# Kernel optimization log

Measured on AMD Instinct MI355X. Metric: run time of the kernel, lower is better.

Reference implementation:

```python
import jax, jax.numpy as jnp
import numpy as np

N_NODES = 20000
N_EDGES = 320000
N_GRAPHS = 64
F_IN = 128
HID = 128
K = 3
LEAK = 0.01  # nn.LeakyReLU default negative_slope


def _glorot(key, shape):
    fan_in, fan_out = shape[-2], shape[-1]
    s = jnp.sqrt(2.0 / (fan_in + fan_out))
    return jax.random.normal(key, shape, dtype=jnp.float32) * s


def setup_inputs() -> dict:
    key = jax.random.key(0)
    ks = jax.random.split(key, 12)
    x = jax.random.normal(ks[0], (N_NODES, F_IN), dtype=jnp.float32)
    edge_index = jax.random.randint(ks[1], (2, N_EDGES), 0, N_NODES, dtype=jnp.int64)
    batch = jnp.sort(jax.random.randint(ks[2], (N_NODES,), 0, N_GRAPHS, dtype=jnp.int64))
    # K-hop GraphConv weights: (K+1) matrices per layer
    W1 = _glorot(ks[3], (K + 1, F_IN, HID));       b1 = jnp.zeros((HID,), jnp.float32)
    W2 = _glorot(ks[4], (K + 1, HID, 2 * HID));    b2 = jnp.zeros((2 * HID,), jnp.float32)
    W3 = _glorot(ks[5], (K + 1, 2 * HID, 4 * HID)); b3 = jnp.zeros((4 * HID,), jnp.float32)
    # classifier MLP
    Wm1 = _glorot(ks[6], (4 * HID, 1024)); bm1 = jnp.zeros((1024,), jnp.float32)
    Wm2 = _glorot(ks[7], (1024, 512));     bm2 = jnp.zeros((512,), jnp.float32)
    Wm3 = _glorot(ks[8], (512, 4));        bm3 = jnp.zeros((4,), jnp.float32)
    return dict(x=x, edge_index=edge_index, batch=batch,
                W1=W1, b1=b1, W2=W2, b2=b2, W3=W3, b3=b3,
                Wm1=Wm1, bm1=bm1, Wm2=Wm2, bm2=bm2, Wm3=Wm3, bm3=bm3)


def _khop_conv(x, src, dst, W, b):
    # out = sum_{k=0..K} (A^k x) W_k + b, A = scatter-sum of src features onto dst
    h = x
    out = h @ W[0]
    for k in range(1, W.shape[0]):
        h = jax.ops.segment_sum(h[src], dst, num_segments=N_NODES)  # one hop
        out = out + h @ W[k]
    return out + b


def reference(x, edge_index, batch, W1, b1, W2, b2, W3, b3, Wm1, bm1, Wm2, bm2, Wm3, bm3):
    src, dst = edge_index[0], edge_index[1]
    h = _khop_conv(x, src, dst, W1, b1)
    h = jnp.where(h > 0, h, LEAK * h)
    h = _khop_conv(h, src, dst, W2, b2)
    h = jnp.where(h > 0, h, LEAK * h)
    h = _khop_conv(h, src, dst, W3, b3)
    # global max pool per graph -> [N_GRAPHS, 4*HID]
    g = jax.ops.segment_max(h, batch, num_segments=N_GRAPHS)
    # classifier head
    g = jax.nn.relu(g @ Wm1 + bm1)
    g = jax.nn.relu(g @ Wm2 + bm2)
    return g @ Wm3 + bm3
```

## Files before the change

kernel.cpp:

```cpp
#include <hip/hip_runtime.h>
#include <stdint.h>

#define NN 20000
#define NNP 20096
#define NE 320000
#define NG 64

typedef unsigned short u16;
typedef __attribute__((ext_vector_type(8))) short short8;
typedef __attribute__((ext_vector_type(4))) float f32x4;

__device__ __forceinline__ void glds16(const void* g, const void* l) {
    __builtin_amdgcn_global_load_lds((const __attribute__((address_space(1))) void*)g,
                                     (__attribute__((address_space(3))) void*)l, 16, 0, 0);
}

__device__ __forceinline__ u16 f2bf(float f) {
    unsigned u = __float_as_uint(f);
    return (u16)((u + 0x7FFFu + ((u >> 16) & 1u)) >> 16);
}

__global__ void hist_kernel(const int* __restrict__ dst, int* __restrict__ cnt, int E) {
    int i = blockIdx.x * blockDim.x + threadIdx.x;
    if (i < E) atomicAdd(&cnt[dst[i]], 1);
}

__global__ void scan_kernel(const int* __restrict__ cnt, int* __restrict__ rp, int n) {
    __shared__ int part[1024];
    int tid = threadIdx.x;
    const int CH = (n + 1023) / 1024;
    int base = tid * CH;
    int s = 0;
    for (int i = 0; i < CH; i++) { int idx = base + i; if (idx < n) s += cnt[idx]; }
    part[tid] = s;
    __syncthreads();
    for (int off = 1; off < 1024; off <<= 1) {
        int v = (tid >= off) ? part[tid - off] : 0;
        __syncthreads();
        part[tid] += v;
        __syncthreads();
    }
    int run = (tid == 0) ? 0 : part[tid - 1];
    for (int i = 0; i < CH; i++) {
        int idx = base + i;
        if (idx < n) { rp[idx] = run; run += cnt[idx]; }
    }
    if (tid == 1023) rp[n] = part[1023];
}

__global__ void copy_int(const int* __restrict__ a, int* __restrict__ b, int n) {
    int i = blockIdx.x * blockDim.x + threadIdx.x;
    if (i < n) b[i] = a[i];
}

__global__ void scatter_kernel(const int* __restrict__ src, const int* __restrict__ dstv,
                               int* __restrict__ ofs, int* __restrict__ col, int E) {
    int i = blockIdx.x * blockDim.x + threadIdx.x;
    if (i < E) {
        int p = atomicAdd(&ofs[dstv[i]], 1);
        col[p] = src[i];
    }
}

__global__ void conv_x(const float* __restrict__ x, u16* __restrict__ S1) {
    int i = blockIdx.x * blockDim.x + threadIdx.x;
    if (i >= NN * 128 / 8) return;
    int row = i >> 4, c = (i & 15) * 8;
    const float* p = x + (size_t)row * 128 + c;
    uint4 r;
    unsigned* pr = (unsigned*)&r;
#pragma unroll
    for (int j = 0; j < 4; j++)
        pr[j] = (unsigned)f2bf(p[2 * j]) | ((unsigned)f2bf(p[2 * j + 1]) << 16);
    *(uint4*)(S1 + (size_t)row * 512 + c) = r;
}

__global__ void convT(const float* __restrict__ W, u16* __restrict__ WT, int K, int M) {
    __shared__ float tile[32][33];
    int m0 = blockIdx.x * 32, k0 = blockIdx.y * 32;
    int tx = threadIdx.x & 31, ty = threadIdx.x >> 5;
#pragma unroll
    for (int i = 0; i < 32; i += 8)
        tile[ty + i][tx] = W[(size_t)(k0 + ty + i) * M + m0 + tx];
    __syncthreads();
#pragma unroll
    for (int i = 0; i < 32; i += 8)
        WT[(size_t)(m0 + ty + i) * K + k0 + tx] = f2bf(tile[tx][ty + i]);
}

__global__ void g2bf(const unsigned* __restrict__ genc, u16* __restrict__ gb) {
    int i = blockIdx.x * blockDim.x + threadIdx.x;
    if (i >= NG * 512) return;
    unsigned u = genc[i];
    u = (u & 0x80000000u) ? (u ^ 0x80000000u) : ~u;
    gb[i] = f2bf(__uint_as_float(u));
}

__global__ __launch_bounds__(256) void prop_win(
    const int* __restrict__ rp, const int* __restrict__ col,
    u16* __restrict__ S, int stride, int in_off, int out_off) {
    int win = blockIdx.x;
    int node = blockIdx.y * 64 + (threadIdx.x >> 2);
    int c = (threadIdx.x & 3) * 8;
    if (node >= NN) return;
    int s0 = rp[node], s1 = rp[node + 1];
    const u16* base = S + in_off + win * 32 + c;
    float acc[8] = {};
    auto accum = [&](uint4 v) {
        const unsigned* pv = (const unsigned*)&v;
#pragma unroll
        for (int j = 0; j < 4; j++) {
            acc[2 * j]     += __uint_as_float(pv[j] << 16);
            acc[2 * j + 1] += __uint_as_float(pv[j] & 0xFFFF0000u);
        }
    };
    int e = s0;
    for (; e + 4 <= s1; e += 4) {
        int i0 = col[e], i1 = col[e + 1], i2 = col[e + 2], i3 = col[e + 3];
        uint4 v0 = *(const uint4*)(base + (size_t)i0 * stride);
        uint4 v1 = *(const uint4*)(base + (size_t)i1 * stride);
        uint4 v2 = *(const uint4*)(base + (size_t)i2 * stride);
        uint4 v3 = *(const uint4*)(base + (size_t)i3 * stride);
        accum(v0); accum(v1); accum(v2); accum(v3);
    }
    for (; e < s1; e++)
        accum(*(const uint4*)(base + (size_t)col[e] * stride));
    uint4 r;
    unsigned* pr = (unsigned*)&r;
#pragma unroll
    for (int j = 0; j < 4; j++)
        pr[j] = (unsigned)f2bf(acc[2 * j]) | ((unsigned)f2bf(acc[2 * j + 1]) << 16);
    *(uint4*)(S + (size_t)node * stride + out_off + win * 32 + c) = r;
}

template <int TM, int EPI, int ACT>
__global__ __launch_bounds__(256) void gemm_bf16(
    const u16* __restrict__ A, int lda, const u16* __restrict__ BT,
    int Kp, int M, const float* __restrict__ bias,
    u16* __restrict__ outB, int ldo,
    unsigned* __restrict__ genc, const int* __restrict__ batch) {
    __shared__ u16 Al[TM * 32];
    __shared__ u16 Bl[128 * 32];
    __shared__ unsigned gbuf[EPI == 1 ? 256 : 4];
    constexpr int MR = TM / 32;
    int col0 = blockIdx.x * 128, row0 = blockIdx.y * TM;
    int t = threadIdx.x;
    int w = t >> 6, ln = t & 63;
    int wm = (w >> 1) * (TM / 2), wn = (w & 1) * 64;
    int srowB = w * 32 + (ln >> 2);
    int srowA = (TM == 128) ? srowB : (w * 16 + (ln >> 2));
    int skc = (ln & 3) * 8;
    f32x4 acc[MR][4] = {};

    if (EPI == 1) gbuf[t] = 0;

    for (int k0 = 0; k0 < Kp; k0 += 32) {
        if (TM == 128) {
            glds16(A + (size_t)(row0 + srowA) * lda + k0 + skc,      &Al[w * 1024]);
            glds16(A + (size_t)(row0 + srowA + 16) * lda + k0 + skc, &Al[w * 1024 + 512]);
        } else {
            glds16(A + (size_t)(row0 + srowA) * lda + k0 + skc,      &Al[w * 512]);
        }
        glds16(BT + (size_t)(col0 + srowB) * Kp + k0 + skc,          &Bl[w * 1024]);
        glds16(BT + (size_t)(col0 + srowB + 16) * Kp + k0 + skc,     &Bl[w * 1024 + 512]);
        __syncthreads();
        short8 af[MR], bf[4];
#pragma unroll
        for (int m = 0; m < MR; m++)
            af[m] = *(const short8*)&Al[(wm + m * 16 + (ln & 15)) * 32 + (ln >> 4) * 8];
#pragma unroll
        for (int n = 0; n < 4; n++)
            bf[n] = *(const short8*)&Bl[(wn + n * 16 + (ln & 15)) * 32 + (ln >> 4) * 8];
#pragma unroll
        for (int m = 0; m < MR; m++)
#pragma unroll
            for (int n = 0; n < 4; n++)
                acc[m][n] = __builtin_amdgcn_mfma_f32_16x16x32_bf16(af[m], bf[n], acc[m][n], 0, 0, 0);
        __syncthreads();
    }

    int g_lo = (EPI == 1) ? batch[row0] : 0;
#pragma unroll
    for (int m = 0; m < MR; m++) {
#pragma unroll
        for (int r = 0; r < 4; r++) {
            int row = row0 + wm + m * 16 + (ln >> 4) * 4 + r;
            if (row < NN) {
                int gb_ = 0, gidx = 0;
                if (EPI == 1) { gb_ = batch[row]; gidx = gb_ - g_lo; }
#pragma unroll
                for (int n = 0; n < 4; n++) {
                    int cl = wn + n * 16 + (ln & 15);
                    float v = acc[m][n][r] + bias[col0 + cl];
                    if (EPI == 0) {
                        v = ACT ? fmaxf(v, 0.f) : (v > 0.f ? v : 0.01f * v);
                        outB[(size_t)row * ldo + col0 + cl] = f2bf(v);
                    } else {
                        unsigned u = __float_as_uint(v);
                        u = (u & 0x80000000u) ? ~u : (u | 0x80000000u);
                        if (gidx < 2) atomicMax(&gbuf[gidx * 128 + cl], u);
                        else          atomicMax(&genc[(size_t)gb_ * M + col0 + cl], u);
                    }
                }
            }
        }
    }
    if (EPI == 1) {
        __syncthreads();
        int j = t >> 7, c = t & 127;
        unsigned u = gbuf[j * 128 + c];
        if (u && g_lo + j < NG) atomicMax(&genc[(size_t)(g_lo + j) * M + col0 + c], u);
    }
}

__global__ void head3(const u16* __restrict__ m2b, const float* __restrict__ W,
                      const float* __restrict__ b, float* __restrict__ outp) {
    int r = blockIdx.x;
    int w = threadIdx.x >> 6;
    int ln = threadIdx.x & 63;
    float acc = 0.f;
    for (int k = ln; k < 512; k += 64) {
        float v = __uint_as_float(((unsigned)m2b[r * 512 + k]) << 16);
        acc += v * W[k * 4 + w];
    }
#pragma unroll
    for (int o = 32; o; o >>= 1) acc += __shfl_down(acc, o, 64);
    if (ln == 0) outp[r * 4 + w] = acc + b[w];
}

extern "C" void kernel_launch(void* const* d_in, const int* in_sizes, int n_in,
                              void* d_out, int out_size, void* d_ws, size_t ws_size,
                              hipStream_t stream) {
    const float* x   = (const float*)d_in[0];
    const int*   ei  = (const int*)d_in[1];
    const int*   bat = (const int*)d_in[2];
    const float* W1  = (const float*)d_in[3];
    const float* b1  = (const float*)d_in[4];
    const float* W2  = (const float*)d_in[5];
    const float* b2  = (const float*)d_in[6];
    const float* W3  = (const float*)d_in[7];
    const float* b3  = (const float*)d_in[8];
    const float* Wm1 = (const float*)d_in[9];
    const float* bm1 = (const float*)d_in[10];
    const float* Wm2 = (const float*)d_in[11];
    const float* bm2 = (const float*)d_in[12];
    const float* Wm3 = (const float*)d_in[13];
    const float* bm3 = (const float*)d_in[14];
    float* out = (float*)d_out;

    char* ws = (char*)d_ws;
    size_t off = 0;
    auto alloc = [&](size_t bytes) -> void* {
        void* p = ws + off;
        off += (bytes + 255) & ~(size_t)255;
        return p;
    };
    int*      cnt  = (int*)alloc((size_t)NN * 4);
    int*      rp   = (int*)alloc((size_t)(NN + 1) * 4);
    int*      col  = (int*)alloc((size_t)NE * 4);
    u16*      S1   = (u16*)alloc((size_t)NNP * 512 * 2);
    u16*      S2   = (u16*)alloc((size_t)NNP * 512 * 2);
    u16*      S3   = (u16*)alloc((size_t)NNP * 1024 * 2);
    u16*      WT1  = (u16*)alloc((size_t)128 * 512 * 2);
    u16*      WT2  = (u16*)alloc((size_t)256 * 512 * 2);
    u16*      WT3  = (u16*)alloc((size_t)512 * 1024 * 2);
    u16*      WTm1 = (u16*)alloc((size_t)1024 * 512 * 2);
    u16*      WTm2 = (u16*)alloc((size_t)512 * 1024 * 2);
    unsigned* genc = (unsigned*)alloc((size_t)NG * 512 * 4);
    u16*      gb   = (u16*)alloc((size_t)NG * 512 * 2);
    u16*      m1b  = (u16*)alloc((size_t)NG * 1024 * 2);
    u16*      m2b  = (u16*)alloc((size_t)NG * 512 * 2);

    const int* src  = ei;
    const int* dstv = ei + NE;

    hipMemsetAsync(cnt, 0, (size_t)NN * 4, stream);
    hist_kernel<<<(NE + 255) / 256, 256, 0, stream>>>(dstv, cnt, NE);
    scan_kernel<<<1, 1024, 0, stream>>>(cnt, rp, NN);
    copy_int<<<(NN + 255) / 256, 256, 0, stream>>>(rp, cnt, NN);
    scatter_kernel<<<(NE + 255) / 256, 256, 0, stream>>>(src, dstv, cnt, col, NE);

    convT<<<dim3(128 / 32, 512 / 32), 256, 0, stream>>>(W1, WT1, 512, 128);
    convT<<<dim3(256 / 32, 512 / 32), 256, 0, stream>>>(W2, WT2, 512, 256);
    convT<<<dim3(512 / 32, 1024 / 32), 256, 0, stream>>>(W3, WT3, 1024, 512);
    convT<<<dim3(1024 / 32, 512 / 32), 256, 0, stream>>>(Wm1, WTm1, 512, 1024);
    convT<<<dim3(512 / 32, 1024 / 32), 256, 0, stream>>>(Wm2, WTm2, 1024, 512);

    conv_x<<<(NN * 16 + 255) / 256, 256, 0, stream>>>(x, S1);

    const int NGY = (NN + 63) / 64;

    prop_win<<<dim3(4, NGY), 256, 0, stream>>>(rp, col, S1, 512, 0, 128);
    prop_win<<<dim3(4, NGY), 256, 0, stream>>>(rp, col, S1, 512, 128, 256);
    prop_win<<<dim3(4, NGY), 256, 0, stream>>>(rp, col, S1, 512, 256, 384);
    gemm_bf16<64, 0, 0><<<dim3(1, NNP / 64), 256, 0, stream>>>(S1, 512, WT1, 512, 128, b1, S2, 512, nullptr, nullptr);

    prop_win<<<dim3(4, NGY), 256, 0, stream>>>(rp, col, S2, 512, 0, 128);
    prop_win<<<dim3(4, NGY), 256, 0, stream>>>(rp, col, S2, 512, 128, 256);
    prop_win<<<dim3(4, NGY), 256, 0, stream>>>(rp, col, S2, 512, 256, 384);
    gemm_bf16<64, 0, 0><<<dim3(2, NNP / 64), 256, 0, stream>>>(S2, 512, WT2, 512, 256, b2, S3, 1024, nullptr, nullptr);

    prop_win<<<dim3(8, NGY), 256, 0, stream>>>(rp, col, S3, 1024, 0, 256);
    prop_win<<<dim3(8, NGY), 256, 0, stream>>>(rp, col, S3, 1024, 256, 512);
    prop_win<<<dim3(8, NGY), 256, 0, stream>>>(rp, col, S3, 1024, 512, 768);
    hipMemsetAsync(genc, 0, (size_t)NG * 512 * 4, stream);
    gemm_bf16<128, 1, 0><<<dim3(4, NNP / 128), 256, 0, stream>>>(S3, 1024, WT3, 1024, 512, b3, nullptr, 0, genc, bat);

    g2bf<<<(NG * 512 + 255) / 256, 256, 0, stream>>>(genc, gb);
    gemm_bf16<64, 0, 1><<<dim3(8, 1), 256, 0, stream>>>(gb, 512, WTm1, 512, 1024, bm1, m1b, 1024, nullptr, nullptr);
    gemm_bf16<64, 0, 1><<<dim3(4, 1), 256, 0, stream>>>(m1b, 1024, WTm2, 1024, 512, bm2, m2b, 512, nullptr, nullptr);
    head3<<<NG, 256, 0, stream>>>(m2b, Wm3, bm3, out);
}
```

Measured before the change: 345.4 us.

## Parallelize neighbor aggregation over edges per node with shared-memory reduction

Replaces the windowed propagation kernel, where each group of four threads walked one node's full edge list for a 32-channel window, with a one-block-per-node kernel. Sixteen edge slots each gather a full 128-channel row, and the partial sums are then reduced across slots through shared memory. The aim is a coalesced full-row gather and better load balance across uneven in-degrees. In exchange it launches 20000 blocks per hop, each with a sync and a serial 16-way reduction. With an average degree near 16, most slots handle about one edge, so most threads sit idle during the reduction.

```diff
diff --git a/kernel.cpp b/kernel.cpp
--- a/kernel.cpp
+++ b/kernel.cpp
@@ -96,41 +96,40 @@
     gb[i] = f2bf(__uint_as_float(u));
 }
 
-__global__ __launch_bounds__(256) void prop_win(
+__global__ __launch_bounds__(256) void prop_epar(
     const int* __restrict__ rp, const int* __restrict__ col,
     u16* __restrict__ S, int stride, int in_off, int out_off) {
-    int win = blockIdx.x;
-    int node = blockIdx.y * 64 + (threadIdx.x >> 2);
-    int c = (threadIdx.x & 3) * 8;
-    if (node >= NN) return;
+    __shared__ float red[16][132];
+    int node = blockIdx.x;
+    int io = in_off + blockIdx.y * 128;
+    int oo = out_off + blockIdx.y * 128;
+    int slot = threadIdx.x >> 4;
+    int ch = threadIdx.x & 15;
     int s0 = rp[node], s1 = rp[node + 1];
-    const u16* base = S + in_off + win * 32 + c;
     float acc[8] = {};
-    auto accum = [&](uint4 v) {
+    const u16* base = S + io + ch * 8;
+    for (int e = s0 + slot; e < s1; e += 16) {
+        int sidx = col[e];
+        uint4 v = *(const uint4*)(base + (size_t)sidx * stride);
         const unsigned* pv = (const unsigned*)&v;
 #pragma unroll
         for (int j = 0; j < 4; j++) {
             acc[2 * j]     += __uint_as_float(pv[j] << 16);
             acc[2 * j + 1] += __uint_as_float(pv[j] & 0xFFFF0000u);
         }
-    };
-    int e = s0;
-    for (; e + 4 <= s1; e += 4) {
-        int i0 = col[e], i1 = col[e + 1], i2 = col[e + 2], i3 = col[e + 3];
-        uint4 v0 = *(const uint4*)(base + (size_t)i0 * stride);
-        uint4 v1 = *(const uint4*)(base + (size_t)i1 * stride);
-        uint4 v2 = *(const uint4*)(base + (size_t)i2 * stride);
-        uint4 v3 = *(const uint4*)(base + (size_t)i3 * stride);
-        accum(v0); accum(v1); accum(v2); accum(v3);
-    }
-    for (; e < s1; e++)
-        accum(*(const uint4*)(base + (size_t)col[e] * stride));
-    uint4 r;
-    unsigned* pr = (unsigned*)&r;
-#pragma unroll
-    for (int j = 0; j < 4; j++)
-        pr[j] = (unsigned)f2bf(acc[2 * j]) | ((unsigned)f2bf(acc[2 * j + 1]) << 16);
-    *(uint4*)(S + (size_t)node * stride + out_off + win * 32 + c) = r;
+    }
+#pragma unroll
+    for (int j = 0; j < 8; j++) red[slot][ch * 8 + j] = acc[j];
+    __syncthreads();
+    int t = threadIdx.x;
+    if (t < 64) {
+        int c0 = t * 2, c1 = t * 2 + 1;
+        float a0 = 0.f, a1 = 0.f;
+#pragma unroll
+        for (int s = 0; s < 16; s++) { a0 += red[s][c0]; a1 += red[s][c1]; }
+        unsigned r = (unsigned)f2bf(a0) | ((unsigned)f2bf(a1) << 16);
+        *(unsigned*)(S + (size_t)node * stride + oo + c0) = r;
+    }
 }
 
 template <int TM, int EPI, int ACT>
@@ -288,21 +287,19 @@
 
     conv_x<<<(NN * 16 + 255) / 256, 256, 0, stream>>>(x, S1);
 
-    const int NGY = (NN + 63) / 64;
-
-    prop_win<<<dim3(4, NGY), 256, 0, stream>>>(rp, col, S1, 512, 0, 128);
-    prop_win<<<dim3(4, NGY), 256, 0, stream>>>(rp, col, S1, 512, 128, 256);
-    prop_win<<<dim3(4, NGY), 256, 0, stream>>>(rp, col, S1, 512, 256, 384);
+    prop_epar<<<dim3(NN, 1), 256, 0, stream>>>(rp, col, S1, 512, 0, 128);
+    prop_epar<<<dim3(NN, 1), 256, 0, stream>>>(rp, col, S1, 512, 128, 256);
+    prop_epar<<<dim3(NN, 1), 256, 0, stream>>>(rp, col, S1, 512, 256, 384);
     gemm_bf16<64, 0, 0><<<dim3(1, NNP / 64), 256, 0, stream>>>(S1, 512, WT1, 512, 128, b1, S2, 512, nullptr, nullptr);
 
-    prop_win<<<dim3(4, NGY), 256, 0, stream>>>(rp, col, S2, 512, 0, 128);
-    prop_win<<<dim3(4, NGY), 256, 0, stream>>>(rp, col, S2, 512, 128, 256);
-    prop_win<<<dim3(4, NGY), 256, 0, stream>>>(rp, col, S2, 512, 256, 384);
+    prop_epar<<<dim3(NN, 1), 256, 0, stream>>>(rp, col, S2, 512, 0, 128);
+    prop_epar<<<dim3(NN, 1), 256, 0, stream>>>(rp, col, S2, 512, 128, 256);
+    prop_epar<<<dim3(NN, 1), 256, 0, stream>>>(rp, col, S2, 512, 256, 384);
     gemm_bf16<64, 0, 0><<<dim3(2, NNP / 64), 256, 0, stream>>>(S2, 512, WT2, 512, 256, b2, S3, 1024, nullptr, nullptr);
 
-    prop_win<<<dim3(8, NGY), 256, 0, stream>>>(rp, col, S3, 1024, 0, 256);
-    prop_win<<<dim3(8, NGY), 256, 0, stream>>>(rp, col, S3, 1024, 256, 512);
-    prop_win<<<dim3(8, NGY), 256, 0, stream>>>(rp, col, S3, 1024, 512, 768);
+    prop_epar<<<dim3(NN, 2), 256, 0, stream>>>(rp, col, S3, 1024, 0, 256);
+    prop_epar<<<dim3(NN, 2), 256, 0, stream>>>(rp, col, S3, 1024, 256, 512);
+    prop_epar<<<dim3(NN, 2), 256, 0, stream>>>(rp, col, S3, 1024, 512, 768);
     hipMemsetAsync(genc, 0, (size_t)NG * 512 * 4, stream);
     gemm_bf16<128, 1, 0><<<dim3(4, NNP / 128), 256, 0, stream>>>(S3, 1024, WT3, 1024, 512, b3, nullptr, 0, genc, bat);
 
```

Result: slower. 410.9 us (+19.0%).
